# Optimization experiments

Hardware: AMD Instinct MI355X
Metric: run time of the kernel (lower is better)

## Reference

```python
import jax, jax.numpy as jnp
import numpy as np

N_HEAD = 16
HEAD_DIM = 64

def setup_inputs() -> dict:
    key = jax.random.key(0)
    k1, k2, k3 = jax.random.split(key, 3)
    B, S, D = 4, 2048, 1024
    x = jax.random.normal(k1, (B, S, D), dtype=jnp.float32)
    mask = jnp.tril(jnp.ones((S, S), dtype=bool))[None, None]  # (1,1,S,S) causal
    w_attn = jax.random.normal(k2, (D, 3 * D), dtype=jnp.float32) * (1.0 / np.sqrt(D))
    b_attn = jnp.zeros((3 * D,), dtype=jnp.float32)
    w_proj = jax.random.normal(k3, (D, D), dtype=jnp.float32) * (1.0 / np.sqrt(D))
    b_proj = jnp.zeros((D,), dtype=jnp.float32)
    return {"x": x, "mask": mask, "w_attn": w_attn, "b_attn": b_attn,
            "w_proj": w_proj, "b_proj": b_proj}

def reference(x, mask, w_attn, b_attn, w_proj, b_proj):
    B, S, D = x.shape
    H, hd = N_HEAD, HEAD_DIM
    qkv = x @ w_attn + b_attn                      # (B,S,3D)
    q, k, v = jnp.split(qkv, 3, axis=-1)
    q = q.reshape(B, S, H, hd).transpose(0, 2, 1, 3)  # (B,H,S,hd)
    k = k.reshape(B, S, H, hd).transpose(0, 2, 1, 3)
    v = v.reshape(B, S, H, hd).transpose(0, 2, 1, 3)
    scores = jnp.einsum('bhqd,bhkd->bhqk', q, k) / jnp.sqrt(jnp.float32(hd))
    scores = jnp.where(mask, scores, jnp.float32(-1e10))
    weights = jax.nn.softmax(scores, axis=-1)      # dropout is identity (deterministic=True)
    attn = jnp.einsum('bhqk,bhkd->bhqd', weights, v)
    attn = attn.transpose(0, 2, 1, 3).reshape(B, S, D)
    return attn @ w_proj + b_proj
```

## Files before the change

### kernel.cpp

```cpp
#include <hip/hip_runtime.h>
#include <hip/hip_bf16.h>
#include <stdint.h>


typedef uint16_t u16;
typedef __bf16 bf16x8 __attribute__((ext_vector_type(8)));
typedef __bf16 bf16x4 __attribute__((ext_vector_type(4)));
typedef short s16x4 __attribute__((ext_vector_type(4)));
typedef float f32x4 __attribute__((ext_vector_type(4)));

#define S_LEN 2048
#define DMODEL 1024
#define NHEAD 16
#define HDIM 64
#define MTOT 8192
#define NQKV 3072
#define QKN 2048

__device__ __forceinline__ u16 f2bf(float f) {
    union { float f; uint32_t u; } v; v.f = f;
    uint32_t u = v.u;
    return (u16)((u + 0x7fffu + ((u >> 16) & 1u)) >> 16);
}

__device__ __forceinline__ s16x4 bits4(bf16x4 v) {
    union { bf16x4 b; s16x4 s; } u; u.b = v; return u.s;
}

__device__ __forceinline__ f32x4 mfma16(bf16x4 a, bf16x4 b, f32x4 c) {
    return __builtin_amdgcn_mfma_f32_16x16x16bf16_1k(bits4(a), bits4(b), c, 0, 0, 0);
}

__device__ __forceinline__ void async_load16(const void* g, void* l) {
    __builtin_amdgcn_global_load_lds(
        (__attribute__((address_space(1))) void*)g,
        (__attribute__((address_space(3))) void*)l,
        16, 0, 0);
}

#define NCONV (MTOT * DMODEL / 4 / 256)
#define NWAT  ((NQKV / 64) * (DMODEL / 64))
#define NWPT  ((DMODEL / 64) * (DMODEL / 64))

__device__ __forceinline__ void transpose_tile(
    const float* __restrict__ in, u16* __restrict__ out, int R, int C,
    int bx, int by, int tid)
{
    __shared__ float tile[64][65];
    int r0 = by * 64, c0 = bx * 64;
    #pragma unroll
    for (int i = 0; i < 16; ++i) {
        int idx = tid + i * 256;
        int r = idx >> 6, c = idx & 63;
        tile[r][c] = in[(size_t)(r0 + r) * C + c0 + c];
    }
    __syncthreads();
    #pragma unroll
    for (int i = 0; i < 16; ++i) {
        int idx = tid + i * 256;
        int c = idx >> 6, r = idx & 63;
        out[(size_t)(c0 + c) * R + r0 + r] = f2bf(tile[r][c]);
    }
}

__global__ void prep_kernel(
    const float4* __restrict__ x4, ushort4* __restrict__ xb4,
    const float* __restrict__ w_attn, u16* __restrict__ wat,
    const float* __restrict__ w_proj, u16* __restrict__ wpt)
{
    const int bid = blockIdx.x;
    const int tid = threadIdx.x;
    if (bid < NCONV) {
        int i = bid * 256 + tid;
        float4 f = x4[i];
        ushort4 o;
        o.x = f2bf(f.x); o.y = f2bf(f.y); o.z = f2bf(f.z); o.w = f2bf(f.w);
        xb4[i] = o;
    } else if (bid < NCONV + NWAT) {
        int b2 = bid - NCONV;
        transpose_tile(w_attn, wat, DMODEL, NQKV, b2 % (NQKV / 64), b2 / (NQKV / 64), tid);
    } else {
        int b3 = bid - NCONV - NWAT;
        transpose_tile(w_proj, wpt, DMODEL, DMODEL, b3 % (DMODEL / 64), b3 / (DMODEL / 64), tid);
    }
}

template<int NF, int OUTMODE>
__global__ __launch_bounds__(512, 2) void gemm16q(
    const u16* __restrict__ A, const u16* __restrict__ Bt,
    const float* __restrict__ bias, void* __restrict__ C,
    u16* __restrict__ vt, int M, int N, int K)
{
    constexpr int NBH = NF / 2;
    constexpr int BSLOT = NF * 4096;
    __shared__ __attribute__((aligned(16))) u16 sm[32768 + 2 * BSLOT];
    u16* const As = sm;
    u16* const Bs = sm + 32768;

    const int tid = threadIdx.x;
    const int wave = tid >> 6, lane = tid & 63;
    const int l15 = lane & 15, q4 = lane >> 4;
    const int wm = wave >> 2, wn = wave & 3;

    const int bid = (int)blockIdx.x;
    const int xcd = bid & 7;
    const int lx  = bid >> 3;
    const int MB  = M >> 8;
    const int PM  = MB >> 3;
    const int nb  = lx / PM;
    const int mb  = xcd * PM + (lx - nb * PM);
    const int m0 = mb << 8, n0 = nb * NF * 64;

    const u16* Ag = A + (size_t)m0 * K;
    const u16* Bg = Bt + (size_t)n0 * K;

    const int srow = tid >> 3;
    const size_t goff0 = (size_t)srow * K + (size_t)(((tid & 7) ^ (srow & 7)) * 8);
    const size_t goff1 = goff0 + (size_t)64 * K;
    const int ldso = tid * 8;

    const int ck0 = (q4 ^ (l15 & 7)) * 8;
    const int ck1 = ((4 + q4) ^ (l15 & 7)) * 8;
    const int rb0 = (wn * NF * 16 + l15) * 64;

    f32x4 acc[8][NF] = {};
    const int T = K >> 6;

#define STAGE_A(t_, h_) do { \
    const u16* ga_ = Ag + (size_t)(h_) * 128 * K + (size_t)(t_) * 64; \
    u16* da_ = As + (((t_) & 1) * 2 + (h_)) * 8192; \
    async_load16(ga_ + goff0, da_ + ldso); \
    async_load16(ga_ + goff1, da_ + ldso + 4096); \
} while (0)

#define STAGE_B(t_, h_) do { \
    const u16* gb_ = Bg + (size_t)(h_) * 128 * K + (size_t)(t_) * 64; \
    u16* db_ = Bs + ((t_) & 1) * BSLOT + (h_) * 8192; \
    async_load16(gb_ + goff0, db_ + ldso); \
    async_load16(gb_ + goff1, db_ + ldso + 4096); \
} while (0)

#define LOAD_AF(P_) do { \
    af[0][0] = *(const bf16x8*)(Ah + ((2 * (P_)) * 16 + l15) * 64 + ck0); \
    af[0][1] = *(const bf16x8*)(Ah + ((2 * (P_)) * 16 + l15) * 64 + ck1); \
    af[1][0] = *(const bf16x8*)(Ah + ((2 * (P_) + 1) * 16 + l15) * 64 + ck0); \
    af[1][1] = *(const bf16x8*)(Ah + ((2 * (P_) + 1) * 16 + l15) * 64 + ck1); \
} while (0)

#define PHASE_MFMA(P_) do { \
    __builtin_amdgcn_s_barrier(); \
    __builtin_amdgcn_s_setprio(1); \
    _Pragma("unroll") \
    for (int i_ = 0; i_ < 2; ++i_) \
        _Pragma("unroll") \
        for (int nf_ = 0; nf_ < NF; ++nf_) \
            _Pragma("unroll") \
            for (int kk_ = 0; kk_ < 2; ++kk_) \
                acc[2 * (P_) + i_][nf_] = __builtin_amdgcn_mfma_f32_16x16x32_bf16( \
                    af[i_][kk_], bfr[nf_][kk_], acc[2 * (P_) + i_][nf_], 0, 0, 0); \
    __builtin_amdgcn_s_setprio(0); \
} while (0)

    STAGE_A(0, 0); STAGE_A(0, 1);
    STAGE_B(0, 0); if constexpr (NBH == 2) STAGE_B(0, 1);
    if (T > 1) {
        STAGE_B(1, 0); if constexpr (NBH == 2) STAGE_B(1, 1);
        if constexpr (NBH == 2) asm volatile("s_waitcnt vmcnt(4)");
        else                    asm volatile("s_waitcnt vmcnt(2)");
    } else {
        asm volatile("s_waitcnt vmcnt(0)");
    }
    __builtin_amdgcn_sched_barrier(0);
    __builtin_amdgcn_s_barrier();

    for (int t = 0; t < T; ++t) {
        const int par = t & 1;
        const u16* Ah = As + (par * 2 + wm) * 8192;
        const u16* Bl = Bs + par * BSLOT;

        bf16x8 af[2][2], bfr[NF][2];

        #pragma unroll
        for (int nf = 0; nf < NF; ++nf) {
            bfr[nf][0] = *(const bf16x8*)(Bl + rb0 + nf * (16 * 64) + ck0);
            bfr[nf][1] = *(const bf16x8*)(Bl + rb0 + nf * (16 * 64) + ck1);
        }
        LOAD_AF(0);
        if (t + 1 < T) STAGE_A(t + 1, 0);
        PHASE_MFMA(0);
        __builtin_amdgcn_s_barrier();

        LOAD_AF(1);
        if (t + 1 < T) STAGE_A(t + 1, 1);
        PHASE_MFMA(1);
        __builtin_amdgcn_s_barrier();

        LOAD_AF(2);
        if (t + 2 < T) STAGE_B(t + 2, 0);
        PHASE_MFMA(2);
        __builtin_amdgcn_s_barrier();

        LOAD_AF(3);
        if constexpr (NBH == 2) { if (t + 2 < T) STAGE_B(t + 2, 1); }
        PHASE_MFMA(3);
        if (t + 1 < T) {
            if (t + 2 < T) {
                if constexpr (NBH == 2) asm volatile("s_waitcnt vmcnt(4)");
                else                    asm volatile("s_waitcnt vmcnt(2)");
            } else {
                asm volatile("s_waitcnt vmcnt(0)");
            }
            __builtin_amdgcn_sched_barrier(0);
            __builtin_amdgcn_s_barrier();
        }
    }

#undef STAGE_A
#undef STAGE_B
#undef LOAD_AF
#undef PHASE_MFMA

    if constexpr (OUTMODE == 1) {
        if (n0 >= 2 * DMODEL && NF == 4) {
            __syncthreads();
            #pragma unroll
            for (int mf = 0; mf < 8; ++mf) {
                #pragma unroll
                for (int nf = 0; nf < NF; ++nf) {
                    const int dp = wn * NF * 16 + nf * 16 + l15;
                    const float bv = bias[n0 + dp];
                    const int g = wm * 32 + mf * 4 + q4;
                    union { __bf16 b[4]; uint2 v; } pk;
                    #pragma unroll
                    for (int r = 0; r < 4; ++r)
                        pk.b[r] = (__bf16)(acc[mf][nf][r] + bv);
                    *(uint2*)&sm[(dp * 64 + (g ^ (dp & 63))) * 4] = pk.v;
                }
            }
            __syncthreads();
            const int b_  = m0 >> 11;
            const int s0  = m0 & (S_LEN - 1);
            const int dv0 = n0 - 2 * DMODEL;
            #pragma unroll
            for (int j = 0; j < 8; ++j) {
                const int dp = wave * 32 + (lane >> 4) + j * 4;
                const int dglob = dv0 + dp;
                const int bh = b_ * NHEAD + (dglob >> 6);
                const int dd = dglob & 63;
                u16* dst = vt + ((size_t)bh * 64 + dd) * S_LEN + s0;
                #pragma unroll
                for (int k = 0; k < 4; ++k) {
                    const int g = l15 + 16 * k;
                    uint2 v = *(const uint2*)&sm[(dp * 64 + (g ^ (dp & 63))) * 4];
                    *(uint2*)&dst[g * 4] = v;
                }
            }
            return;
        }
    }

    #pragma unroll
    for (int mf = 0; mf < 8; ++mf) {
        const int row = m0 + wm * 128 + mf * 16 + q4 * 4;
        #pragma unroll
        for (int nf = 0; nf < NF; ++nf) {
            const int col = n0 + wn * NF * 16 + nf * 16 + l15;
            const float bv = bias[col];
            if constexpr (OUTMODE == 0) {
                #pragma unroll
                for (int r = 0; r < 4; ++r)
                    ((float*)C)[(size_t)(row + r) * N + col] = acc[mf][nf][r] + bv;
            } else {
                #pragma unroll
                for (int r = 0; r < 4; ++r)
                    ((u16*)C)[(size_t)(row + r) * QKN + col] = f2bf(acc[mf][nf][r] + bv);
            }
        }
    }
}

__device__ __forceinline__ void stage_tiles(
    const u16* __restrict__ qk, const u16* __restrict__ vt,
    size_t base, int bh, int h, int w, int srow8, int schunk,
    int kt, u16* __restrict__ KsB, u16* __restrict__ VsB)
{
    #pragma unroll
    for (int q = 0; q < 2; ++q) {
        int rloc = w * 16 + q * 8 + srow8;
        int sc = ((schunk ^ (rloc & 7)) * 8);
        async_load16(qk + (base + (size_t)kt * 64 + rloc) * (size_t)QKN + DMODEL + h * HDIM + sc,
                     KsB + (w * 16 + q * 8) * 64);
        async_load16(vt + ((size_t)bh * 64 + rloc) * S_LEN + kt * 64 + sc,
                     VsB + (w * 16 + q * 8) * 64);
    }
}

__device__ __forceinline__ void attn_pass(
    int qt, const u16* __restrict__ qk, const u16* __restrict__ vt,
    __bf16* __restrict__ outb, u16 (*Ks)[64 * 64], u16 (*Vs)[64 * 64],
    int w, int lane, int bh, int h, size_t base)
{
    const int l15 = lane & 15, q4 = lane >> 4;
    const int srow8 = lane >> 3, schunk = lane & 7;

    const float QSCALE = 0.125f * 1.44269504f;
    bf16x8 qf[2][2];
    #pragma unroll
    for (int mh = 0; mh < 2; ++mh) {
        int qrow = qt * 128 + mh * 64 + w * 16 + l15;
        #pragma unroll
        for (int kc = 0; kc < 2; ++kc) {
            bf16x8 raw = *(const bf16x8*)(qk + (base + qrow) * (size_t)QKN + h * HDIM + kc * 32 + q4 * 8);
            bf16x8 sc;
            #pragma unroll
            for (int j = 0; j < 8; ++j) sc[j] = (__bf16)((float)raw[j] * QSCALE);
            qf[mh][kc] = sc;
        }
    }

    bf16x4 ones4;
    #pragma unroll
    for (int j = 0; j < 4; ++j) ones4[j] = (__bf16)1.0f;

    f32x4 o0[4] = {}, o1[4] = {};
    f32x4 la0 = {}, la1 = {};

    const int ktlast = 2 * qt + 1;

    __syncthreads();
    stage_tiles(qk, vt, base, bh, h, w, srow8, schunk, 0, Ks[0], Vs[0]);
    if (ktlast >= 1)
        stage_tiles(qk, vt, base, bh, h, w, srow8, schunk, 1, Ks[1], Vs[1]);

    for (int kt = 0; kt <= 2 * qt; ++kt) {
        const int buf = kt % 3;
        __syncthreads();
        int pf = kt + 2;
        if (pf <= ktlast)
            stage_tiles(qk, vt, base, bh, h, w, srow8, schunk, pf, Ks[pf % 3], Vs[pf % 3]);

        f32x4 st0[4] = {}, st1[4] = {};
        #pragma unroll
        for (int nt = 0; nt < 4; ++nt) {
            int n = nt * 16 + l15;
            #pragma unroll
            for (int kc = 0; kc < 2; ++kc) {
                int ch = (((kc * 4 + q4) ^ (n & 7)) * 8);
                bf16x8 kf = *(const bf16x8*)(&Ks[buf][n * 64 + ch]);
                st0[nt] = __builtin_amdgcn_mfma_f32_16x16x32_bf16(kf, qf[0][kc], st0[nt], 0, 0, 0);
                st1[nt] = __builtin_amdgcn_mfma_f32_16x16x32_bf16(kf, qf[1][kc], st1[nt], 0, 0, 0);
            }
        }

        if (kt == 2 * qt) {
            #pragma unroll
            for (int nt = 0; nt < 4; ++nt)
                #pragma unroll
                for (int r = 0; r < 4; ++r) {
                    int keyl = nt * 16 + q4 * 4 + r;
                    if (keyl > w * 16 + l15) st0[nt][r] = -1e30f;
                }
        }

        bf16x4 pb0[4], pb1[4];
        #pragma unroll
        for (int nt = 0; nt < 4; ++nt)
            #pragma unroll
            for (int r = 0; r < 4; ++r) {
                pb0[nt][r] = (__bf16)__builtin_amdgcn_exp2f(st0[nt][r]);
                pb1[nt][r] = (__bf16)__builtin_amdgcn_exp2f(st1[nt][r]);
            }

        #pragma unroll
        for (int nt = 0; nt < 4; ++nt) {
            #pragma unroll
            for (int mt = 0; mt < 4; ++mt) {
                int row = mt * 16 + l15;
                int ch = (nt * 2 + (q4 >> 1)) ^ (row & 7);
                bf16x4 vf = *(const bf16x4*)(&Vs[buf][row * 64 + ch * 8 + (q4 & 1) * 4]);
                o0[mt] = mfma16(vf, pb0[nt], o0[mt]);
                o1[mt] = mfma16(vf, pb1[nt], o1[mt]);
            }
            la0 = mfma16(ones4, pb0[nt], la0);
            la1 = mfma16(ones4, pb1[nt], la1);
        }
    }

    {
        const int buf = ktlast % 3;
        __syncthreads();

        f32x4 st1[4] = {};
        #pragma unroll
        for (int nt = 0; nt < 4; ++nt) {
            int n = nt * 16 + l15;
            #pragma unroll
            for (int kc = 0; kc < 2; ++kc) {
                int ch = (((kc * 4 + q4) ^ (n & 7)) * 8);
                bf16x8 kf = *(const bf16x8*)(&Ks[buf][n * 64 + ch]);
                st1[nt] = __builtin_amdgcn_mfma_f32_16x16x32_bf16(kf, qf[1][kc], st1[nt], 0, 0, 0);
            }
        }
        bf16x4 pb1[4];
        #pragma unroll
        for (int nt = 0; nt < 4; ++nt)
            #pragma unroll
            for (int r = 0; r < 4; ++r) {
                int keyl = nt * 16 + q4 * 4 + r;
                float s = (keyl > w * 16 + l15) ? -1e30f : st1[nt][r];
                pb1[nt][r] = (__bf16)__builtin_amdgcn_exp2f(s);
            }
        #pragma unroll
        for (int nt = 0; nt < 4; ++nt) {
            #pragma unroll
            for (int mt = 0; mt < 4; ++mt) {
                int row = mt * 16 + l15;
                int ch = (nt * 2 + (q4 >> 1)) ^ (row & 7);
                bf16x4 vf = *(const bf16x4*)(&Vs[buf][row * 64 + ch * 8 + (q4 & 1) * 4]);
                o1[mt] = mfma16(vf, pb1[nt], o1[mt]);
            }
            la1 = mfma16(ones4, pb1[nt], la1);
        }
    }

    float inv0 = 1.0f / la0[0], inv1 = 1.0f / la1[0];
    int row0 = qt * 128 + w * 16 + l15;
    int row1 = row0 + 64;
    #pragma unroll
    for (int mt = 0; mt < 4; ++mt) {
        union { __bf16 b[4]; ushort4 v; } p0, p1;
        #pragma unroll
        for (int r = 0; r < 4; ++r) {
            p0.b[r] = (__bf16)(o0[mt][r] * inv0);
            p1.b[r] = (__bf16)(o1[mt][r] * inv1);
        }
        int col = h * HDIM + mt * 16 + q4 * 4;
        *(ushort4*)(&outb[(base + row0) * (size_t)DMODEL + col]) = p0.v;
        *(ushort4*)(&outb[(base + row1) * (size_t)DMODEL + col]) = p1.v;
    }
}

__global__ __launch_bounds__(256, 3) void attn_kernel(
    const u16* __restrict__ qk, const u16* __restrict__ vt, u16* __restrict__ out)
{
    __shared__ __attribute__((aligned(16))) u16 Ks[3][64 * 64];
    __shared__ __attribute__((aligned(16))) u16 Vs[3][64 * 64];

    const int tid = threadIdx.x;
    const int w = tid >> 6, lane = tid & 63;
    const int bh = blockIdx.y;
    const int b = bh >> 4, h = bh & 15;
    const size_t base = (size_t)b * S_LEN;
    const int NT = (int)gridDim.x * 2;

    attn_pass(NT - 1 - (int)blockIdx.x, qk, vt, (__bf16*)out, Ks, Vs, w, lane, bh, h, base);
    attn_pass((int)blockIdx.x,          qk, vt, (__bf16*)out, Ks, Vs, w, lane, bh, h, base);
}

extern "C" void kernel_launch(void* const* d_in, const int* in_sizes, int n_in,
                              void* d_out, int out_size, void* d_ws, size_t ws_size,
                              hipStream_t stream) {
    const float* x      = (const float*)d_in[0];
    const float* w_attn = (const float*)d_in[2];
    const float* b_attn = (const float*)d_in[3];
    const float* w_proj = (const float*)d_in[4];
    const float* b_proj = (const float*)d_in[5];

    u16* xb   = (u16*)d_ws;
    u16* wat  = xb  + (size_t)MTOT * DMODEL;
    u16* wpt  = wat + (size_t)NQKV * DMODEL;
    u16* qk   = wpt + (size_t)DMODEL * DMODEL;
    u16* vt   = qk  + (size_t)MTOT * QKN;
    u16* attn = vt  + (size_t)64 * 64 * S_LEN;

    prep_kernel<<<NCONV + NWAT + NWPT, 256, 0, stream>>>(
        (const float4*)x, (ushort4*)xb, w_attn, wat, w_proj, wpt);

    gemm16q<4, 1><<<dim3((MTOT / 256) * (NQKV / 256)), 512, 0, stream>>>(
        xb, wat, b_attn, (void*)qk, vt, MTOT, NQKV, DMODEL);

    attn_kernel<<<dim3(S_LEN / 256, 4 * NHEAD), 256, 0, stream>>>(qk, vt, attn);

    gemm16q<2, 0><<<dim3((MTOT / 256) * (DMODEL / 128)), 512, 0, stream>>>(
        attn, wpt, b_proj, d_out, nullptr, MTOT, DMODEL, DMODEL);
}
```

Before: 255.8 us.

## Replace pipelined 256-row GEMM with simple 128x128 single-buffered GEMM

```diff
diff --git a/kernel.cpp b/kernel.cpp
--- a/kernel.cpp
+++ b/kernel.cpp
@@ -85,156 +85,77 @@
     }
 }
 
-template<int NF, int OUTMODE>
-__global__ __launch_bounds__(512, 2) void gemm16q(
+template<int OUTMODE>
+__global__ __launch_bounds__(256, 3) void gemm_bt(
     const u16* __restrict__ A, const u16* __restrict__ Bt,
     const float* __restrict__ bias, void* __restrict__ C,
     u16* __restrict__ vt, int M, int N, int K)
 {
-    constexpr int NBH = NF / 2;
-    constexpr int BSLOT = NF * 4096;
-    __shared__ __attribute__((aligned(16))) u16 sm[32768 + 2 * BSLOT];
+    __shared__ __attribute__((aligned(16))) u16 sm[16384];
     u16* const As = sm;
-    u16* const Bs = sm + 32768;
+    u16* const Bs = sm + 4096;
 
     const int tid = threadIdx.x;
     const int wave = tid >> 6, lane = tid & 63;
     const int l15 = lane & 15, q4 = lane >> 4;
-    const int wm = wave >> 2, wn = wave & 3;
+    const int wm = wave >> 1, wn = wave & 1;
 
     const int bid = (int)blockIdx.x;
     const int xcd = bid & 7;
     const int lx  = bid >> 3;
-    const int MB  = M >> 8;
-    const int PM  = MB >> 3;
-    const int nb  = lx / PM;
-    const int mb  = xcd * PM + (lx - nb * PM);
-    const int m0 = mb << 8, n0 = nb * NF * 64;
+    const int nb  = lx >> 3;
+    const int mb  = xcd * 8 + (lx & 7);
+    const int m0 = mb << 7, n0 = nb << 7;
 
     const u16* Ag = A + (size_t)m0 * K;
     const u16* Bg = Bt + (size_t)n0 * K;
 
-    const int srow = tid >> 3;
-    const size_t goff0 = (size_t)srow * K + (size_t)(((tid & 7) ^ (srow & 7)) * 8);
-    const size_t goff1 = goff0 + (size_t)64 * K;
-    const int ldso = tid * 8;
-
-    const int ck0 = (q4 ^ (l15 & 7)) * 8;
-    const int ck1 = ((4 + q4) ^ (l15 & 7)) * 8;
-    const int rb0 = (wn * NF * 16 + l15) * 64;
-
-    f32x4 acc[8][NF] = {};
-    const int T = K >> 6;
-
-#define STAGE_A(t_, h_) do { \
-    const u16* ga_ = Ag + (size_t)(h_) * 128 * K + (size_t)(t_) * 64; \
-    u16* da_ = As + (((t_) & 1) * 2 + (h_)) * 8192; \
-    async_load16(ga_ + goff0, da_ + ldso); \
-    async_load16(ga_ + goff1, da_ + ldso + 4096); \
-} while (0)
-
-#define STAGE_B(t_, h_) do { \
-    const u16* gb_ = Bg + (size_t)(h_) * 128 * K + (size_t)(t_) * 64; \
-    u16* db_ = Bs + ((t_) & 1) * BSLOT + (h_) * 8192; \
-    async_load16(gb_ + goff0, db_ + ldso); \
-    async_load16(gb_ + goff1, db_ + ldso + 4096); \
-} while (0)
-
-#define LOAD_AF(P_) do { \
-    af[0][0] = *(const bf16x8*)(Ah + ((2 * (P_)) * 16 + l15) * 64 + ck0); \
-    af[0][1] = *(const bf16x8*)(Ah + ((2 * (P_)) * 16 + l15) * 64 + ck1); \
-    af[1][0] = *(const bf16x8*)(Ah + ((2 * (P_) + 1) * 16 + l15) * 64 + ck0); \
-    af[1][1] = *(const bf16x8*)(Ah + ((2 * (P_) + 1) * 16 + l15) * 64 + ck1); \
-} while (0)
-
-#define PHASE_MFMA(P_) do { \
-    __builtin_amdgcn_s_barrier(); \
-    __builtin_amdgcn_s_setprio(1); \
-    _Pragma("unroll") \
-    for (int i_ = 0; i_ < 2; ++i_) \
-        _Pragma("unroll") \
-        for (int nf_ = 0; nf_ < NF; ++nf_) \
-            _Pragma("unroll") \
-            for (int kk_ = 0; kk_ < 2; ++kk_) \
-                acc[2 * (P_) + i_][nf_] = __builtin_amdgcn_mfma_f32_16x16x32_bf16( \
-                    af[i_][kk_], bfr[nf_][kk_], acc[2 * (P_) + i_][nf_], 0, 0, 0); \
-    __builtin_amdgcn_s_setprio(0); \
-} while (0)
-
-    STAGE_A(0, 0); STAGE_A(0, 1);
-    STAGE_B(0, 0); if constexpr (NBH == 2) STAGE_B(0, 1);
-    if (T > 1) {
-        STAGE_B(1, 0); if constexpr (NBH == 2) STAGE_B(1, 1);
-        if constexpr (NBH == 2) asm volatile("s_waitcnt vmcnt(4)");
-        else                    asm volatile("s_waitcnt vmcnt(2)");
-    } else {
-        asm volatile("s_waitcnt vmcnt(0)");
-    }
-    __builtin_amdgcn_sched_barrier(0);
-    __builtin_amdgcn_s_barrier();
-
-    for (int t = 0; t < T; ++t) {
-        const int par = t & 1;
-        const u16* Ah = As + (par * 2 + wm) * 8192;
-        const u16* Bl = Bs + par * BSLOT;
-
-        bf16x8 af[2][2], bfr[NF][2];
-
-        #pragma unroll
-        for (int nf = 0; nf < NF; ++nf) {
-            bfr[nf][0] = *(const bf16x8*)(Bl + rb0 + nf * (16 * 64) + ck0);
-            bfr[nf][1] = *(const bf16x8*)(Bl + rb0 + nf * (16 * 64) + ck1);
-        }
-        LOAD_AF(0);
-        if (t + 1 < T) STAGE_A(t + 1, 0);
-        PHASE_MFMA(0);
-        __builtin_amdgcn_s_barrier();
-
-        LOAD_AF(1);
-        if (t + 1 < T) STAGE_A(t + 1, 1);
-        PHASE_MFMA(1);
-        __builtin_amdgcn_s_barrier();
-
-        LOAD_AF(2);
-        if (t + 2 < T) STAGE_B(t + 2, 0);
-        PHASE_MFMA(2);
-        __builtin_amdgcn_s_barrier();
-
-        LOAD_AF(3);
-        if constexpr (NBH == 2) { if (t + 2 < T) STAGE_B(t + 2, 1); }
-        PHASE_MFMA(3);
-        if (t + 1 < T) {
-            if (t + 2 < T) {
-                if constexpr (NBH == 2) asm volatile("s_waitcnt vmcnt(4)");
-                else                    asm volatile("s_waitcnt vmcnt(2)");
-            } else {
-                asm volatile("s_waitcnt vmcnt(0)");
-            }
-            __builtin_amdgcn_sched_barrier(0);
-            __builtin_amdgcn_s_barrier();
-        }
-    }
-
-#undef STAGE_A
-#undef STAGE_B
-#undef LOAD_AF
-#undef PHASE_MFMA
+    const int l3 = lane >> 3;
+    const int sch = (lane & 7) ^ l3;
+    const int srow = wave * 32 + 2 * l3 + (sch >> 2);
+    const int scol = (sch & 3) * 8;
+    const int ldst = (wave * 32) * 32;
+
+    const int ck = (l15 >> 1) * 64 + ((((l15 & 1) * 4 + q4) ^ (l15 >> 1)) * 8);
+
+    f32x4 acc[4][4] = {};
+
+    for (int k0 = 0; k0 < K; k0 += 32) {
+        #pragma unroll
+        for (int q = 0; q < 2; ++q) {
+            async_load16(Ag + (size_t)(srow + q * 16) * K + k0 + scol, As + ldst + q * 512);
+            async_load16(Bg + (size_t)(srow + q * 16) * K + k0 + scol, Bs + ldst + q * 512);
+        }
+        __syncthreads();
+
+        bf16x8 af[4], bfr[4];
+        #pragma unroll
+        for (int t = 0; t < 4; ++t) {
+            af[t]  = *(const bf16x8*)(As + wm * 2048 + t * 512 + ck);
+            bfr[t] = *(const bf16x8*)(Bs + wn * 2048 + t * 512 + ck);
+        }
+        #pragma unroll
+        for (int tm = 0; tm < 4; ++tm)
+            #pragma unroll
+            for (int tn = 0; tn < 4; ++tn)
+                acc[tm][tn] = __builtin_amdgcn_mfma_f32_16x16x32_bf16(af[tm], bfr[tn], acc[tm][tn], 0, 0, 0);
+        __syncthreads();
+    }
 
     if constexpr (OUTMODE == 1) {
-        if (n0 >= 2 * DMODEL && NF == 4) {
-            __syncthreads();
-            #pragma unroll
-            for (int mf = 0; mf < 8; ++mf) {
+        if (n0 >= 2 * DMODEL) {
+            #pragma unroll
+            for (int tm = 0; tm < 4; ++tm) {
+                const int g = wm * 16 + tm * 4 + q4;
                 #pragma unroll
-                for (int nf = 0; nf < NF; ++nf) {
-                    const int dp = wn * NF * 16 + nf * 16 + l15;
+                for (int tn = 0; tn < 4; ++tn) {
+                    const int dp = wn * 64 + tn * 16 + l15;
                     const float bv = bias[n0 + dp];
-                    const int g = wm * 32 + mf * 4 + q4;
                     union { __bf16 b[4]; uint2 v; } pk;
                     #pragma unroll
                     for (int r = 0; r < 4; ++r)
-                        pk.b[r] = (__bf16)(acc[mf][nf][r] + bv);
-                    *(uint2*)&sm[(dp * 64 + (g ^ (dp & 63))) * 4] = pk.v;
+                        pk.b[r] = (__bf16)(acc[tm][tn][r] + bv);
+                    *(uint2*)&sm[(dp * 32 + (g ^ (dp & 31))) * 4] = pk.v;
                 }
             }
             __syncthreads();
@@ -243,15 +164,15 @@
             const int dv0 = n0 - 2 * DMODEL;
             #pragma unroll
             for (int j = 0; j < 8; ++j) {
-                const int dp = wave * 32 + (lane >> 4) + j * 4;
+                const int dp = wave * 32 + q4 * 8 + j;
                 const int dglob = dv0 + dp;
                 const int bh = b_ * NHEAD + (dglob >> 6);
                 const int dd = dglob & 63;
                 u16* dst = vt + ((size_t)bh * 64 + dd) * S_LEN + s0;
                 #pragma unroll
-                for (int k = 0; k < 4; ++k) {
+                for (int k = 0; k < 2; ++k) {
                     const int g = l15 + 16 * k;
-                    uint2 v = *(const uint2*)&sm[(dp * 64 + (g ^ (dp & 63))) * 4];
+                    uint2 v = *(const uint2*)&sm[(dp * 32 + (g ^ (dp & 31))) * 4];
                     *(uint2*)&dst[g * 4] = v;
                 }
             }
@@ -260,20 +181,20 @@
     }
 
     #pragma unroll
-    for (int mf = 0; mf < 8; ++mf) {
-        const int row = m0 + wm * 128 + mf * 16 + q4 * 4;
-        #pragma unroll
-        for (int nf = 0; nf < NF; ++nf) {
-            const int col = n0 + wn * NF * 16 + nf * 16 + l15;
+    for (int tm = 0; tm < 4; ++tm) {
+        const int row = m0 + wm * 64 + tm * 16 + q4 * 4;
+        #pragma unroll
+        for (int tn = 0; tn < 4; ++tn) {
+            const int col = n0 + wn * 64 + tn * 16 + l15;
             const float bv = bias[col];
             if constexpr (OUTMODE == 0) {
                 #pragma unroll
                 for (int r = 0; r < 4; ++r)
-                    ((float*)C)[(size_t)(row + r) * N + col] = acc[mf][nf][r] + bv;
+                    ((float*)C)[(size_t)(row + r) * N + col] = acc[tm][tn][r] + bv;
             } else {
                 #pragma unroll
                 for (int r = 0; r < 4; ++r)
-                    ((u16*)C)[(size_t)(row + r) * QKN + col] = f2bf(acc[mf][nf][r] + bv);
+                    ((u16*)C)[(size_t)(row + r) * QKN + col] = f2bf(acc[tm][tn][r] + bv);
             }
         }
     }
@@ -476,11 +397,11 @@
     prep_kernel<<<NCONV + NWAT + NWPT, 256, 0, stream>>>(
         (const float4*)x, (ushort4*)xb, w_attn, wat, w_proj, wpt);
 
-    gemm16q<4, 1><<<dim3((MTOT / 256) * (NQKV / 256)), 512, 0, stream>>>(
+    gemm_bt<1><<<dim3((MTOT / 128) * (NQKV / 128)), 256, 0, stream>>>(
         xb, wat, b_attn, (void*)qk, vt, MTOT, NQKV, DMODEL);
 
     attn_kernel<<<dim3(S_LEN / 256, 4 * NHEAD), 256, 0, stream>>>(qk, vt, attn);
 
-    gemm16q<2, 0><<<dim3((MTOT / 256) * (DMODEL / 128)), 512, 0, stream>>>(
+    gemm_bt<0><<<dim3((MTOT / 128) * (DMODEL / 128)), 256, 0, stream>>>(
         attn, wpt, b_proj, d_out, nullptr, MTOT, DMODEL, DMODEL);
 }
```

Result: no change. 255.6 us (-0.1%).
